# Kernel tuning notes

Measured on AMD Instinct MI355X. Metric: run time of the kernel, lower is better.

The kernel has to match this reference:

```python
import jax, jax.numpy as jnp
import numpy as np

B, N, C = 4, 1024, 768          # batch, tokens, embed_dim
D, H, HD, FF = 12, 12, 64, 3072  # depth, heads, head_dim, mlp hidden
LN_EPS = 1e-5


def setup_inputs() -> dict:
    key = jax.random.key(0)
    ks = jax.random.split(key, 12)
    w = lambda i, shape: jax.random.normal(ks[i], shape, jnp.float32) * 0.02
    return {
        "x": jax.random.normal(ks[0], (B, N, C), jnp.float32),
        "pos_x": jax.random.normal(ks[1], (B, N, C), jnp.float32),
        # stacked per-layer params (leading dim D)
        "qkv_w": w(2, (D, 3 * C, C)), "qkv_b": w(3, (D, 3 * C)),
        "proj_w": w(4, (D, C, C)),    "proj_b": w(5, (D, C)),
        "fc1_w": w(6, (D, FF, C)),    "fc1_b": w(7, (D, FF)),
        "fc2_w": w(8, (D, C, FF)),    "fc2_b": w(9, (D, C)),
        "ln1_g": jnp.ones((D, C), jnp.float32), "ln1_b": jnp.zeros((D, C), jnp.float32),
        "ln2_g": jnp.ones((D, C), jnp.float32), "ln2_b": jnp.zeros((D, C), jnp.float32),
        "normf_g": jnp.ones((C,), jnp.float32), "normf_b": jnp.zeros((C,), jnp.float32),
    }


def _ln(x, g, b):
    mu = jnp.mean(x, axis=-1, keepdims=True)
    var = jnp.mean((x - mu) ** 2, axis=-1, keepdims=True)
    return (x - mu) * jax.lax.rsqrt(var + LN_EPS) * g + b


def reference(x, pos_x, qkv_w, qkv_b, proj_w, proj_b, fc1_w, fc1_b, fc2_w, fc2_b,
              ln1_g, ln1_b, ln2_g, ln2_b, normf_g, normf_b):
    scale = 1.0 / jnp.sqrt(jnp.float32(HD))
    x = x + pos_x  # pos added once (add_pos_at_every_layer=False)

    def block(xc, p):
        qw, qb, pw, pb, f1w, f1b, f2w, f2b, g1, b1, g2, b2 = p
        h = _ln(xc, g1, b1)
        qkv = jnp.einsum('bnc,oc->bno', h, qw) + qb            # [B,N,3C]
        qkv = qkv.reshape(B, N, 3, H, HD).transpose(2, 0, 3, 1, 4)
        q, k, v = qkv[0], qkv[1], qkv[2]                       # [B,H,N,HD]
        attn = jax.nn.softmax(jnp.einsum('bhnd,bhmd->bhnm', q, k) * scale, axis=-1)
        o = jnp.einsum('bhnm,bhmd->bhnd', attn, v)
        o = o.transpose(0, 2, 1, 3).reshape(B, N, C)
        xc = xc + (jnp.einsum('bnc,oc->bno', o, pw) + pb)      # residual + proj
        h2 = _ln(xc, g2, b2)
        hid = jax.nn.gelu(jnp.einsum('bnc,fc->bnf', h2, f1w) + f1b, approximate=False)
        ffn = jnp.einsum('bnf,of->bno', hid, f2w) + f2b
        xc = xc + ffn
        return xc, None

    xs = (qkv_w, qkv_b, proj_w, proj_b, fc1_w, fc1_b, fc2_w, fc2_b,
          ln1_g, ln1_b, ln2_g, ln2_b)
    x, _ = jax.lax.scan(block, x, xs)
    return _ln(x, normf_g, normf_b)  # postnorm
```

## Files before the change

kernel.cpp:

```cpp
#include <hip/hip_runtime.h>
#include <hip/hip_bf16.h>
#include <math.h>

typedef __bf16 bf16;
typedef __bf16 bf16x8 __attribute__((ext_vector_type(8)));
typedef __bf16 bf16x4 __attribute__((ext_vector_type(4)));
typedef float  f32x4  __attribute__((ext_vector_type(4)));

#define B_  4
#define N_  1024
#define C_  768
#define H_  12
#define HD_ 64
#define FF_ 3072
#define T_  (B_*N_)
#define D_  12

__device__ __forceinline__ void gld_lds16(const void* g, void* l) {
    __builtin_amdgcn_global_load_lds(
        (const __attribute__((address_space(1))) void*)g,
        (__attribute__((address_space(3))) void*)l, 16, 0, 0);
}

__device__ __forceinline__ float gelu_f(float v) {
    const float ax = fabsf(v) * 0.70710678118f;
    const float t  = __frcp_rn(1.0f + 0.3275911f * ax);
    float p = 1.061405429f;
    p = p * t - 1.453152027f;
    p = p * t + 1.421413741f;
    p = p * t - 0.284496736f;
    p = p * t + 0.254829592f;
    const float e = p * t * __expf(-ax * ax);
    const float erfv = (v >= 0.f) ? (1.0f - e) : (e - 1.0f);
    return 0.5f * v * (1.0f + erfv);
}

template<typename WT, int MODE>
__global__ __launch_bounds__(256) void gemm_bt(
    const bf16* __restrict__ A, const WT* __restrict__ Bt,
    const float* __restrict__ bias, bf16* __restrict__ out,
    float* __restrict__ resid, int M, int N, int Kfull, int Ks)
{
    __shared__ __align__(16) bf16 lA[64*64];
    __shared__ __align__(16) WT   lB[128*64];
    const int tid  = threadIdx.x;
    const int lane = tid & 63, wave = tid >> 6;
    const int lo = lane & 15, hi = lane >> 4;
    const int wm = wave & 1, wn = wave >> 1;

    const int nblk = gridDim.x;
    const int id2  = (blockIdx.x & 7) * (nblk >> 3) + (blockIdx.x >> 3);
    const int gx = M >> 6, gy = N >> 7;
    const int bx  = id2 % gx;
    const int byz = id2 / gx;
    const int by  = byz % gy;
    const int bz  = byz / gy;
    const int row0 = bx * 64, col0 = by * 128;
    const int k0base = bz * Ks;

    f32x4 acc[2][4];
#pragma unroll
    for (int i = 0; i < 2; i++)
#pragma unroll
        for (int j = 0; j < 4; j++) acc[i][j] = (f32x4){0.f, 0.f, 0.f, 0.f};

    for (int k0 = k0base; k0 < k0base + Ks; k0 += 64) {
#pragma unroll
        for (int r = 0; r < 2; ++r) {
            const int cb    = r * 256 + wave * 64;
            const int chunk = cb + lane;
            const int rw = chunk >> 3, kc = chunk & 7;
            const int kcs = kc ^ (rw & 7);
            gld_lds16(A + (size_t)(row0 + rw) * Kfull + k0 + kcs * 8, lA + cb * 8);
        }
        if constexpr (sizeof(WT) == 2) {
#pragma unroll
            for (int r = 0; r < 4; ++r) {
                const int cb    = r * 256 + wave * 64;
                const int chunk = cb + lane;
                const int rw = chunk >> 3, kc = chunk & 7;
                const int kcs = kc ^ (rw & 7);
                gld_lds16(Bt + (size_t)(col0 + rw) * Kfull + k0 + kcs * 8,
                          (bf16*)lB + cb * 8);
            }
        } else {
#pragma unroll
            for (int r = 0; r < 8; ++r) {
                const int cb    = r * 256 + wave * 64;
                const int chunk = cb + lane;
                const int rw = chunk >> 4, kc = chunk & 15;
                const int kcs = kc ^ ((rw & 7) << 1);
                gld_lds16(Bt + (size_t)(col0 + rw) * Kfull + k0 + kcs * 4,
                          (float*)lB + cb * 4);
            }
        }
        __syncthreads();
#pragma unroll 1
        for (int s = 0; s < 2; ++s) {
            bf16x8 af[2], bfr[4];
#pragma unroll
            for (int i = 0; i < 2; i++) {
                const int rowA = wm * 32 + i * 16 + lo;
                const int ca = (s * 4 + hi) ^ (lo & 7);
                af[i] = *(const bf16x8*)(lA + rowA * 64 + ca * 8);
            }
#pragma unroll
            for (int i = 0; i < 4; i++) {
                const int rowB = wn * 64 + i * 16 + lo;
                if constexpr (sizeof(WT) == 2) {
                    const int cc = (s * 4 + hi) ^ (lo & 7);
                    bfr[i] = *(const bf16x8*)((const bf16*)lB + rowB * 64 + cc * 8);
                } else {
                    const float* base = (const float*)lB + rowB * 64;
                    const int c0 = (s * 8 + hi * 2) ^ ((lo & 7) << 1);
                    const f32x4 u0 = *(const f32x4*)(base + c0 * 4);
                    const f32x4 u1 = *(const f32x4*)(base + (c0 + 1) * 4);
                    bf16x8 f;
#pragma unroll
                    for (int e = 0; e < 4; e++) { f[e] = (bf16)u0[e]; f[4+e] = (bf16)u1[e]; }
                    bfr[i] = f;
                }
            }
#pragma unroll
            for (int mi = 0; mi < 2; mi++)
#pragma unroll
                for (int ni = 0; ni < 4; ni++)
                    acc[mi][ni] = __builtin_amdgcn_mfma_f32_16x16x32_bf16(
                        af[mi], bfr[ni], acc[mi][ni], 0, 0, 0);
        }
        __syncthreads();
    }

    const float bscale = (bz == 0) ? 1.0f : 0.0f;
#pragma unroll
    for (int mi = 0; mi < 2; mi++) {
#pragma unroll
        for (int ni = 0; ni < 4; ni++) {
            const int gcol = col0 + wn * 64 + ni * 16 + lo;
            const float bv = bias[gcol] * bscale;
#pragma unroll
            for (int r = 0; r < 4; r++) {
                const int grow = row0 + wm * 32 + mi * 16 + hi * 4 + r;
                float v = acc[mi][ni][r] + bv;
                if (MODE == 1) v = gelu_f(v);
                if (MODE == 2) {
                    atomicAdd(&resid[(size_t)grow * N + gcol], v);
                } else {
                    out[(size_t)grow * N + gcol] = (bf16)v;
                }
            }
        }
    }
}

__global__ __launch_bounds__(256) void cvt_k(
    const float* __restrict__ src, bf16* __restrict__ dst)
{
    const int i = (blockIdx.x * 256 + threadIdx.x) * 8;
    const f32x4 a = *(const f32x4*)(src + i);
    const f32x4 b = *(const f32x4*)(src + i + 4);
    bf16x8 o;
#pragma unroll
    for (int e = 0; e < 4; e++) { o[e] = (bf16)a[e]; o[4 + e] = (bf16)b[e]; }
    *(bf16x8*)(dst + i) = o;
}

template<typename OutT>
__global__ __launch_bounds__(256) void ln_k(
    const float* __restrict__ x, const float* __restrict__ g,
    const float* __restrict__ b, OutT* __restrict__ out)
{
    const int wave = threadIdx.x >> 6, lane = threadIdx.x & 63;
    const int t = blockIdx.x * 4 + wave;
    const float* row = x + (size_t)t * C_;
    f32x4 v[3];
    float s = 0.f, ss = 0.f;
#pragma unroll
    for (int j = 0; j < 3; j++) {
        v[j] = *(const f32x4*)(row + (j * 64 + lane) * 4);
#pragma unroll
        for (int e = 0; e < 4; e++) { s += v[j][e]; ss += v[j][e] * v[j][e]; }
    }
#pragma unroll
    for (int off = 32; off > 0; off >>= 1) {
        s  += __shfl_xor(s, off);
        ss += __shfl_xor(ss, off);
    }
    const float mu  = s * (1.f / 768.f);
    const float var = ss * (1.f / 768.f) - mu * mu;
    const float rs  = rsqrtf(var + 1e-5f);
    OutT* orow = out + (size_t)t * C_;
#pragma unroll
    for (int j = 0; j < 3; j++) {
        const f32x4 gv = *(const f32x4*)(g + (j * 64 + lane) * 4);
        const f32x4 bv = *(const f32x4*)(b + (j * 64 + lane) * 4);
#pragma unroll
        for (int e = 0; e < 4; e++)
            orow[(j * 64 + lane) * 4 + e] = (OutT)((v[j][e] - mu) * rs * gv[e] + bv[e]);
    }
}

__global__ __launch_bounds__(256) void addpos_k(
    const float* __restrict__ x, const float* __restrict__ p, float* __restrict__ o)
{
    const int i = (blockIdx.x * 256 + threadIdx.x) * 4;
    const f32x4 xv = *(const f32x4*)(x + i);
    const f32x4 pv = *(const f32x4*)(p + i);
    f32x4 ov;
#pragma unroll
    for (int e = 0; e < 4; e++) ov[e] = xv[e] + pv[e];
    *(f32x4*)(o + i) = ov;
}

#define SKD_ 72
#define SVK_ 136
#define SPK_ 136
__global__ __launch_bounds__(256) void attn_k(
    const bf16* __restrict__ qkv, bf16* __restrict__ out)
{
    const int id2 = (blockIdx.x & 7) * 96 + (blockIdx.x >> 3);
    const int qt = id2 & 15;
    const int bh = id2 >> 4;
    const int b = bh / H_, h = bh % H_;
    const int lane = threadIdx.x & 63, wave = threadIdx.x >> 6;
    const int lo = lane & 15, hi = lane >> 4;

    __shared__ __align__(16) bf16 lK[128 * SKD_];
    __shared__ __align__(16) bf16 lV[64 * SVK_];
    __shared__ __align__(16) bf16 lP[4][16 * SPK_];

    const size_t tokbase = (size_t)b * N_;

    const bf16* qptr = qkv + (tokbase + qt * 64 + wave * 16 + lo) * (3 * C_) + h * HD_;
    bf16x8 qf0 = *(const bf16x8*)(qptr + hi * 8);
    bf16x8 qf1 = *(const bf16x8*)(qptr + 32 + hi * 8);
#pragma unroll
    for (int e = 0; e < 8; e++) {
        qf0[e] = (bf16)((float)qf0[e] * 0.125f);
        qf1[e] = (bf16)((float)qf1[e] * 0.125f);
    }

    float m_r[4], l_r[4];
    f32x4 oacc[4];
#pragma unroll
    for (int r = 0; r < 4; r++) { m_r[r] = -1e30f; l_r[r] = 0.f; }
#pragma unroll
    for (int di = 0; di < 4; di++) oacc[di] = (f32x4){0.f, 0.f, 0.f, 0.f};

    for (int kt = 0; kt < 8; ++kt) {
        const int kb0 = kt * 128;
#pragma unroll
        for (int r = 0; r < 4; ++r) {
            const int chunk = r * 256 + threadIdx.x;
            const int key = chunk >> 3, dc = chunk & 7;
            const bf16* kp = qkv + (tokbase + kb0 + key) * (3 * C_) + C_ + h * HD_ + dc * 8;
            *(bf16x8*)(lK + key * SKD_ + dc * 8) = *(const bf16x8*)kp;
        }
#pragma unroll
        for (int r = 0; r < 4; ++r) {
            const int chunk = r * 256 + threadIdx.x;
            const int d = chunk & 63, kg = chunk >> 6;
            const bf16* vp = qkv + (tokbase + kb0 + kg * 8) * (3 * C_)
                           + 2 * C_ + h * HD_ + d;
            bf16x8 tv;
#pragma unroll
            for (int i = 0; i < 8; i++) tv[i] = vp[(size_t)i * (3 * C_)];
            *(bf16x8*)(lV + d * SVK_ + kg * 8) = tv;
        }
        __syncthreads();

        f32x4 sacc[8];
#pragma unroll
        for (int kb = 0; kb < 8; kb++) {
            const bf16x8 b0 = *(const bf16x8*)(lK + (kb * 16 + lo) * SKD_ + hi * 8);
            const bf16x8 b1 = *(const bf16x8*)(lK + (kb * 16 + lo) * SKD_ + 32 + hi * 8);
            f32x4 a = (f32x4){0.f, 0.f, 0.f, 0.f};
            a = __builtin_amdgcn_mfma_f32_16x16x32_bf16(qf0, b0, a, 0, 0, 0);
            a = __builtin_amdgcn_mfma_f32_16x16x32_bf16(qf1, b1, a, 0, 0, 0);
            sacc[kb] = a;
        }

        float pm[4], mn[4], ts[4];
#pragma unroll
        for (int r = 0; r < 4; r++) {
            float a0 = fmaxf(fmaxf(sacc[0][r], sacc[1][r]),
                             fmaxf(sacc[2][r], sacc[3][r]));
            float a1 = fmaxf(fmaxf(sacc[4][r], sacc[5][r]),
                             fmaxf(sacc[6][r], sacc[7][r]));
            pm[r] = fmaxf(a0, a1);
            ts[r] = 0.f;
        }
        const int okd = (pm[0] <= m_r[0] + 8.f) && (pm[1] <= m_r[1] + 8.f)
                     && (pm[2] <= m_r[2] + 8.f) && (pm[3] <= m_r[3] + 8.f);
        const bool defer = __all(okd);
        if (defer) {
#pragma unroll
            for (int r = 0; r < 4; r++) mn[r] = m_r[r];
        } else {
#pragma unroll
            for (int r = 0; r < 4; r++) {
                float tm = pm[r];
#pragma unroll
                for (int off = 1; off < 16; off <<= 1)
                    tm = fmaxf(tm, __shfl_xor(tm, off));
                mn[r] = fmaxf(m_r[r], tm);
            }
        }
#pragma unroll
        for (int kb = 0; kb < 8; kb++)
#pragma unroll
            for (int r = 0; r < 4; r++) {
                const float p = __expf(sacc[kb][r] - mn[r]);
                lP[wave][(hi * 4 + r) * SPK_ + kb * 16 + lo] = (bf16)p;
                ts[r] += p;
            }
#pragma unroll
        for (int r = 0; r < 4; r++)
#pragma unroll
            for (int off = 1; off < 16; off <<= 1)
                ts[r] += __shfl_xor(ts[r], off);
        if (defer) {
#pragma unroll
            for (int r = 0; r < 4; r++) l_r[r] += ts[r];
        } else {
            float alpha[4];
#pragma unroll
            for (int r = 0; r < 4; r++) {
                alpha[r] = __expf(m_r[r] - mn[r]);
                l_r[r] = l_r[r] * alpha[r] + ts[r];
                m_r[r] = mn[r];
            }
#pragma unroll
            for (int di = 0; di < 4; di++)
#pragma unroll
                for (int r = 0; r < 4; r++) oacc[di][r] *= alpha[r];
        }

        bf16x8 pa[4];
#pragma unroll
        for (int s = 0; s < 4; s++)
            pa[s] = *(const bf16x8*)(&lP[wave][lo * SPK_ + s * 32 + hi * 8]);
#pragma unroll
        for (int di = 0; di < 4; di++) {
#pragma unroll
            for (int s = 0; s < 4; s++) {
                const bf16x8 v = *(const bf16x8*)(lV + (di * 16 + lo) * SVK_ + s * 32 + hi * 8);
                oacc[di] = __builtin_amdgcn_mfma_f32_16x16x32_bf16(pa[s], v, oacc[di], 0, 0, 0);
            }
        }
        __syncthreads();
    }

    float il[4];
#pragma unroll
    for (int r = 0; r < 4; r++) il[r] = 1.0f / l_r[r];
#pragma unroll
    for (int di = 0; di < 4; di++)
#pragma unroll
        for (int r = 0; r < 4; r++) {
            const size_t tok = tokbase + qt * 64 + wave * 16 + hi * 4 + r;
            out[tok * C_ + h * HD_ + di * 16 + lo] = (bf16)(oacc[di][r] * il[r]);
        }
}

extern "C" void kernel_launch(void* const* d_in, const int* in_sizes, int n_in,
                              void* d_out, int out_size, void* d_ws, size_t ws_size,
                              hipStream_t stream)
{
    const float* x      = (const float*)d_in[0];
    const float* pos_x  = (const float*)d_in[1];
    const float* qkv_w  = (const float*)d_in[2];
    const float* qkv_b  = (const float*)d_in[3];
    const float* proj_w = (const float*)d_in[4];
    const float* proj_b = (const float*)d_in[5];
    const float* fc1_w  = (const float*)d_in[6];
    const float* fc1_b  = (const float*)d_in[7];
    const float* fc2_w  = (const float*)d_in[8];
    const float* fc2_b  = (const float*)d_in[9];
    const float* ln1_g  = (const float*)d_in[10];
    const float* ln1_b  = (const float*)d_in[11];
    const float* ln2_g  = (const float*)d_in[12];
    const float* ln2_b  = (const float*)d_in[13];
    const float* nf_g   = (const float*)d_in[14];
    const float* nf_b   = (const float*)d_in[15];

    char* ws = (char*)d_ws;
    float* xres  = (float*)(ws);
    bf16* hbuf   = (bf16*)(ws + 12582912);
    bf16* qkvbuf = (bf16*)(ws + 18874368);
    bf16* attno  = (bf16*)(ws + 37748736);
    bf16* hid    = (bf16*)(ws + 44040192);
    bf16* wq     = (bf16*)(ws + 69206016);
    bf16* wp     = (bf16*)(ws + 111673344);
    bf16* w1     = (bf16*)(ws + 125829120);
    bf16* w2     = (bf16*)(ws + 182452224);
    const bool usebf16 = ws_size >= (size_t)239075328;

    addpos_k<<<T_ * C_ / 4 / 256, 256, 0, stream>>>(x, pos_x, xres);

    if (usebf16) {
        cvt_k<<<D_ * 3 * C_ * C_ / 2048, 256, 0, stream>>>(qkv_w, wq);
        cvt_k<<<D_ * C_ * C_ / 2048, 256, 0, stream>>>(proj_w, wp);
        cvt_k<<<D_ * FF_ * C_ / 2048, 256, 0, stream>>>(fc1_w, w1);
        cvt_k<<<D_ * C_ * FF_ / 2048, 256, 0, stream>>>(fc2_w, w2);
    }

    const int g_qkv  = (T_/64) * ((3*C_)/128);
    const int g_proj = (T_/64) * (C_/128) * 2;
    const int g_fc1  = (T_/64) * (FF_/128);
    const int g_fc2  = (T_/64) * (C_/128) * 2;

    for (int L = 0; L < D_; ++L) {
        ln_k<bf16><<<T_ / 4, 256, 0, stream>>>(xres, ln1_g + L * C_, ln1_b + L * C_, hbuf);
        if (usebf16) {
            gemm_bt<bf16,0><<<g_qkv, 256, 0, stream>>>(
                hbuf, wq + (size_t)L * 3 * C_ * C_, qkv_b + (size_t)L * 3 * C_,
                qkvbuf, nullptr, T_, 3 * C_, C_, C_);
        } else {
            gemm_bt<float,0><<<g_qkv, 256, 0, stream>>>(
                hbuf, qkv_w + (size_t)L * 3 * C_ * C_, qkv_b + (size_t)L * 3 * C_,
                qkvbuf, nullptr, T_, 3 * C_, C_, C_);
        }
        attn_k<<<N_ / 64 * B_ * H_, 256, 0, stream>>>(qkvbuf, attno);
        if (usebf16) {
            gemm_bt<bf16,2><<<g_proj, 256, 0, stream>>>(
                attno, wp + (size_t)L * C_ * C_, proj_b + (size_t)L * C_,
                nullptr, xres, T_, C_, C_, C_ / 2);
        } else {
            gemm_bt<float,2><<<g_proj, 256, 0, stream>>>(
                attno, proj_w + (size_t)L * C_ * C_, proj_b + (size_t)L * C_,
                nullptr, xres, T_, C_, C_, C_ / 2);
        }
        ln_k<bf16><<<T_ / 4, 256, 0, stream>>>(xres, ln2_g + L * C_, ln2_b + L * C_, hbuf);
        if (usebf16) {
            gemm_bt<bf16,1><<<g_fc1, 256, 0, stream>>>(
                hbuf, w1 + (size_t)L * FF_ * C_, fc1_b + (size_t)L * FF_,
                hid, nullptr, T_, FF_, C_, C_);
            gemm_bt<bf16,2><<<g_fc2, 256, 0, stream>>>(
                hid, w2 + (size_t)L * C_ * FF_, fc2_b + (size_t)L * C_,
                nullptr, xres, T_, C_, FF_, FF_ / 2);
        } else {
            gemm_bt<float,1><<<g_fc1, 256, 0, stream>>>(
                hbuf, fc1_w + (size_t)L * FF_ * C_, fc1_b + (size_t)L * FF_,
                hid, nullptr, T_, FF_, C_, C_);
            gemm_bt<float,2><<<g_fc2, 256, 0, stream>>>(
                hid, fc2_w + (size_t)L * C_ * FF_, fc2_b + (size_t)L * C_,
                nullptr, xres, T_, C_, FF_, FF_ / 2);
        }
    }
    ln_k<float><<<T_ / 4, 256, 0, stream>>>(xres, nf_g, nf_b, (float*)d_out);
}
```

Before: 2.591 ms.

## Double-buffer bf16 GEMM tiles with register-staged prefetch

For bf16 weights, the GEMM main loop switches from direct global-to-LDS loads to a register-staged software pipeline with two LDS buffers. Tile t+2 is loaded into registers and tile t+1 is written to the other buffer while tile t is computed, leaving one barrier per iteration. This aims to hide global load latency behind MFMA work, at the cost of extra registers and doubled LDS use, which may reduce occupancy. The fp32-weight path is kept single-buffered.

```diff
diff --git a/kernel.cpp b/kernel.cpp
--- a/kernel.cpp
+++ b/kernel.cpp
@@ -21,6 +21,13 @@
         (const __attribute__((address_space(1))) void*)g,
         (__attribute__((address_space(3))) void*)l, 16, 0, 0);
 }
+
+#define SEAL() do {                                         \
+    asm volatile("s_waitcnt lgkmcnt(0)" ::: "memory");      \
+    __builtin_amdgcn_sched_barrier(0);                      \
+    __builtin_amdgcn_s_barrier();                           \
+    __builtin_amdgcn_sched_barrier(0);                      \
+} while (0)
 
 __device__ __forceinline__ float gelu_f(float v) {
     const float ax = fabsf(v) * 0.70710678118f;
@@ -41,8 +48,10 @@
     const float* __restrict__ bias, bf16* __restrict__ out,
     float* __restrict__ resid, int M, int N, int Kfull, int Ks)
 {
-    __shared__ __align__(16) bf16 lA[64*64];
-    __shared__ __align__(16) WT   lB[128*64];
+    constexpr bool BF = (sizeof(WT) == 2);
+    constexpr int NB  = BF ? 2 : 1;
+    __shared__ __align__(16) bf16 lA[NB][64*64];
+    __shared__ __align__(16) WT   lB[NB][128*64];
     const int tid  = threadIdx.x;
     const int lane = tid & 63, wave = tid >> 6;
     const int lo = lane & 15, hi = lane >> 4;
@@ -57,6 +66,7 @@
     const int bz  = byz / gy;
     const int row0 = bx * 64, col0 = by * 128;
     const int k0base = bz * Ks;
+    const int nt = Ks >> 6;
 
     f32x4 acc[2][4];
 #pragma unroll
@@ -64,54 +74,110 @@
 #pragma unroll
         for (int j = 0; j < 4; j++) acc[i][j] = (f32x4){0.f, 0.f, 0.f, 0.f};
 
-    for (int k0 = k0base; k0 < k0base + Ks; k0 += 64) {
+    if constexpr (BF) {
+        const bf16* pA[2]; int wAo[2];
 #pragma unroll
         for (int r = 0; r < 2; ++r) {
-            const int cb    = r * 256 + wave * 64;
-            const int chunk = cb + lane;
-            const int rw = chunk >> 3, kc = chunk & 7;
-            const int kcs = kc ^ (rw & 7);
-            gld_lds16(A + (size_t)(row0 + rw) * Kfull + k0 + kcs * 8, lA + cb * 8);
-        }
-        if constexpr (sizeof(WT) == 2) {
-#pragma unroll
-            for (int r = 0; r < 4; ++r) {
+            const int c = tid + r * 256;
+            const int rw = c >> 3, kc = c & 7;
+            pA[r]  = A + (size_t)(row0 + rw) * Kfull + k0base + kc * 8;
+            wAo[r] = rw * 64 + (kc ^ (rw & 7)) * 8;
+        }
+        const bf16* pB[4]; int wBo[4];
+#pragma unroll
+        for (int r = 0; r < 4; ++r) {
+            const int c = tid + r * 256;
+            const int rw = c >> 3, kc = c & 7;
+            pB[r]  = (const bf16*)Bt + (size_t)(col0 + rw) * Kfull + k0base + kc * 8;
+            wBo[r] = rw * 64 + (kc ^ (rw & 7)) * 8;
+        }
+        bf16x8 rA[2], rB[4];
+        auto loadT = [&](int t) {
+#pragma unroll
+            for (int r = 0; r < 2; ++r) rA[r] = *(const bf16x8*)(pA[r] + t * 64);
+#pragma unroll
+            for (int r = 0; r < 4; ++r) rB[r] = *(const bf16x8*)(pB[r] + t * 64);
+        };
+        auto writeT = [&](int buf) {
+#pragma unroll
+            for (int r = 0; r < 2; ++r) *(bf16x8*)(&lA[buf][wAo[r]]) = rA[r];
+#pragma unroll
+            for (int r = 0; r < 4; ++r) *(bf16x8*)(&((bf16*)lB[buf])[wBo[r]]) = rB[r];
+        };
+        auto compute = [&](int buf) {
+#pragma unroll 1
+            for (int s = 0; s < 2; ++s) {
+                bf16x8 af[2], bfr[4];
+#pragma unroll
+                for (int i = 0; i < 2; i++) {
+                    const int rowA = wm * 32 + i * 16 + lo;
+                    const int ca = (s * 4 + hi) ^ (lo & 7);
+                    af[i] = *(const bf16x8*)(&lA[buf][rowA * 64 + ca * 8]);
+                }
+#pragma unroll
+                for (int i = 0; i < 4; i++) {
+                    const int rowB = wn * 64 + i * 16 + lo;
+                    const int cc = (s * 4 + hi) ^ (lo & 7);
+                    bfr[i] = *(const bf16x8*)(&((const bf16*)lB[buf])[rowB * 64 + cc * 8]);
+                }
+#pragma unroll
+                for (int mi = 0; mi < 2; mi++)
+#pragma unroll
+                    for (int ni = 0; ni < 4; ni++)
+                        acc[mi][ni] = __builtin_amdgcn_mfma_f32_16x16x32_bf16(
+                            af[mi], bfr[ni], acc[mi][ni], 0, 0, 0);
+            }
+        };
+
+        loadT(0);
+        writeT(0);
+        if (nt > 1) loadT(1);
+        SEAL();
+        int cur = 0;
+#pragma unroll 1
+        for (int t = 0; t < nt; ++t) {
+            if (t + 1 < nt) {
+                writeT(cur ^ 1);
+                if (t + 2 < nt) loadT(t + 2);
+            }
+            compute(cur);
+            SEAL();
+            cur ^= 1;
+        }
+    } else {
+        for (int t = 0; t < nt; ++t) {
+#pragma unroll
+            for (int r = 0; r < 2; ++r) {
                 const int cb    = r * 256 + wave * 64;
                 const int chunk = cb + lane;
                 const int rw = chunk >> 3, kc = chunk & 7;
                 const int kcs = kc ^ (rw & 7);
-                gld_lds16(Bt + (size_t)(col0 + rw) * Kfull + k0 + kcs * 8,
-                          (bf16*)lB + cb * 8);
-            }
-        } else {
+                gld_lds16(A + (size_t)(row0 + rw) * Kfull + k0base + t * 64 + kcs * 8,
+                          lA[0] + cb * 8);
+            }
 #pragma unroll
             for (int r = 0; r < 8; ++r) {
                 const int cb    = r * 256 + wave * 64;
                 const int chunk = cb + lane;
                 const int rw = chunk >> 4, kc = chunk & 15;
                 const int kcs = kc ^ ((rw & 7) << 1);
-                gld_lds16(Bt + (size_t)(col0 + rw) * Kfull + k0 + kcs * 4,
-                          (float*)lB + cb * 4);
-            }
-        }
-        __syncthreads();
+                gld_lds16(Bt + (size_t)(col0 + rw) * Kfull + k0base + t * 64 + kcs * 4,
+                          (float*)lB[0] + cb * 4);
+            }
+            __syncthreads();
 #pragma unroll 1
-        for (int s = 0; s < 2; ++s) {
-            bf16x8 af[2], bfr[4];
-#pragma unroll
-            for (int i = 0; i < 2; i++) {
-                const int rowA = wm * 32 + i * 16 + lo;
-                const int ca = (s * 4 + hi) ^ (lo & 7);
-                af[i] = *(const bf16x8*)(lA + rowA * 64 + ca * 8);
-            }
-#pragma unroll
-            for (int i = 0; i < 4; i++) {
-                const int rowB = wn * 64 + i * 16 + lo;
-                if constexpr (sizeof(WT) == 2) {
-                    const int cc = (s * 4 + hi) ^ (lo & 7);
-                    bfr[i] = *(const bf16x8*)((const bf16*)lB + rowB * 64 + cc * 8);
-                } else {
-                    const float* base = (const float*)lB + rowB * 64;
+            for (int s = 0; s < 2; ++s) {
+                bf16x8 af[2], bfr[4];
+#pragma unroll
+                for (int i = 0; i < 2; i++) {
+                    const int rowA = wm * 32 + i * 16 + lo;
+                    const int ca = (s * 4 + hi) ^ (lo & 7);
+                    af[i] = *(const bf16x8*)(&lA[0][rowA * 64 + ca * 8]);
+                }
+#pragma unroll
+                for (int i = 0; i < 4; i++) {
+                    const int rowB = wn * 64 + i * 16 + lo;
+                    const float* base = (const float*)lB[0] + rowB * 64;
                     const int c0 = (s * 8 + hi * 2) ^ ((lo & 7) << 1);
                     const f32x4 u0 = *(const f32x4*)(base + c0 * 4);
                     const f32x4 u1 = *(const f32x4*)(base + (c0 + 1) * 4);
@@ -120,15 +186,15 @@
                     for (int e = 0; e < 4; e++) { f[e] = (bf16)u0[e]; f[4+e] = (bf16)u1[e]; }
                     bfr[i] = f;
                 }
-            }
-#pragma unroll
-            for (int mi = 0; mi < 2; mi++)
-#pragma unroll
-                for (int ni = 0; ni < 4; ni++)
-                    acc[mi][ni] = __builtin_amdgcn_mfma_f32_16x16x32_bf16(
-                        af[mi], bfr[ni], acc[mi][ni], 0, 0, 0);
-        }
-        __syncthreads();
+#pragma unroll
+                for (int mi = 0; mi < 2; mi++)
+#pragma unroll
+                    for (int ni = 0; ni < 4; ni++)
+                        acc[mi][ni] = __builtin_amdgcn_mfma_f32_16x16x32_bf16(
+                            af[mi], bfr[ni], acc[mi][ni], 0, 0, 0);
+            }
+            __syncthreads();
+        }
     }
 
     const float bscale = (bz == 0) ? 1.0f : 0.0f;
```

Result: faster. 2.512 ms (-3.0%).
